# Kernel optimization log

Hardware: AMD Instinct MI355X
Metric: run time of the kernel (lower is better)

The kernel has to match this reference:

```python
import jax, jax.numpy as jnp
import numpy as np

T, N, E = 8, 20000, 320000
D_IN, H, OUT = 64, 128, 2
EPS = 1e-5  # BatchNorm eps


def setup_inputs() -> dict:
    key = jax.random.key(0)
    ks = jax.random.split(key, 24)
    rn = lambda k, shape: jax.random.normal(k, shape, jnp.float32) * 0.05
    inp = {
        "x_seq": jax.random.normal(ks[0], (T, N, D_IN), jnp.float32),
        "edge_index_seq": jax.random.randint(ks[1], (T, 2, E), 0, N),
        # GCN layer 1 (D_IN -> H) + BatchNorm (eval mode: running stats)
        "W1": rn(ks[2], (D_IN, H)), "b1": jnp.zeros((H,), jnp.float32),
        "g1": jnp.ones((H,), jnp.float32), "be1": jnp.zeros((H,), jnp.float32),
        "m1": rn(ks[3], (H,)), "v1": jax.random.uniform(ks[4], (H,), jnp.float32, 0.5, 1.5),
        # GCN layer 2 (H -> H) + BatchNorm
        "W2": rn(ks[5], (H, H)), "b2": jnp.zeros((H,), jnp.float32),
        "g2": jnp.ones((H,), jnp.float32), "be2": jnp.zeros((H,), jnp.float32),
        "m2": rn(ks[6], (H,)), "v2": jax.random.uniform(ks[7], (H,), jnp.float32, 0.5, 1.5),
        # LSTM layer 0 (PyTorch layout: W_ih [4H, in], W_hh [4H, H], gate order i,f,g,o)
        "Wih0": rn(ks[8], (4 * H, H)), "Whh0": rn(ks[9], (4 * H, H)),
        "bih0": jnp.zeros((4 * H,), jnp.float32), "bhh0": jnp.zeros((4 * H,), jnp.float32),
        # LSTM layer 1
        "Wih1": rn(ks[10], (4 * H, H)), "Whh1": rn(ks[11], (4 * H, H)),
        "bih1": jnp.zeros((4 * H,), jnp.float32), "bhh1": jnp.zeros((4 * H,), jnp.float32),
        # final classifier
        "Wc": rn(ks[12], (OUT, H)), "bc": jnp.zeros((OUT,), jnp.float32),
    }
    return inp


def gcn_conv(x, src, dst, W, b):
    # GCNConv: D^{-1/2}(A+I)D^{-1/2} X W + b, self-loops added
    n = x.shape[0]
    h = x @ W                                   # [N, F_out]
    loop = jnp.arange(n)
    s = jnp.concatenate([src, loop])
    d = jnp.concatenate([dst, loop])
    deg = jax.ops.segment_sum(jnp.ones(d.shape, x.dtype), d, num_segments=n)
    dinv = jax.lax.rsqrt(deg)                   # deg >= 1 (self-loops)
    coef = dinv[s] * dinv[d]                    # [E+N]
    agg = jax.ops.segment_sum(h[s] * coef[:, None], d, num_segments=n)
    return agg + b


def batchnorm_eval(x, g, b, m, v):
    return (x - m) * jax.lax.rsqrt(v + EPS) * g + b


def lstm_layer(xs, Wih, Whh, b):
    # xs: [T, in]; returns (ys [T,H], h_T [H])
    h0 = jnp.zeros((Whh.shape[1],), xs.dtype)

    def step(carry, xt):
        h, c = carry
        gates = xt @ Wih.T + h @ Whh.T + b
        i, f, g, o = jnp.split(gates, 4, axis=-1)
        c = jax.nn.sigmoid(f) * c + jax.nn.sigmoid(i) * jnp.tanh(g)
        h = jax.nn.sigmoid(o) * jnp.tanh(c)
        return (h, c), h

    (hT, _), ys = jax.lax.scan(step, (h0, h0), xs)
    return ys, hT


def reference(x_seq, edge_index_seq, W1, b1, g1, be1, m1, v1,
              W2, b2, g2, be2, m2, v2,
              Wih0, Whh0, bih0, bhh0, Wih1, Whh1, bih1, bhh1, Wc, bc):
    def per_t(x, e):
        src, dst = e[0], e[1]
        h = gcn_conv(x, src, dst, W1, b1)
        h = jax.nn.relu(batchnorm_eval(h, g1, be1, m1, v1))
        h = gcn_conv(h, src, dst, W2, b2)
        h = batchnorm_eval(h, g2, be2, m2, v2)
        return h.mean(axis=0)                   # global mean pool (batch=None)

    emb = jax.vmap(per_t)(x_seq, edge_index_seq)  # [T, H]
    ys, _ = lstm_layer(emb, Wih0, Whh0, bih0 + bhh0)
    _, hT = lstm_layer(ys, Wih1, Whh1, bih1 + bhh1)
    out = hT @ Wc.T + bc                          # [OUT]
    return (out[None, :], hT[None, :])
```

## Files before the change

kernel.cpp:

```cpp
#include <hip/hip_runtime.h>
#include <hip/hip_fp16.h>
#include <math.h>

#define T 8
#define N 20000
#define E 320000
#define EPS 1e-5f
#define NBA 32
#define CHUNKA 10000
#define NPACK 10000
#define NPACK4 5000
#define TILES_PT 1250
#define BW 625
#define NBUK 32
#define SPAN_MAX 13824
#define CSGRID 157
#define CVTBLK 2500

typedef _Float16 f16x8 __attribute__((ext_vector_type(8)));
typedef float f32x4 __attribute__((ext_vector_type(4)));
struct h2x2 { __half2 lo, hi; };

__device__ __forceinline__ float sigm(float x) { return 1.0f / (1.0f + expf(-x)); }

__global__ __launch_bounds__(1024) void k_partA(const int* __restrict__ edges,
                                                unsigned int* __restrict__ hist_g,
                                                unsigned int* __restrict__ bpart,
                                                int* __restrict__ bcnt) {
    __shared__ unsigned int arr[CHUNKA];
    __shared__ int cnt[NBUK], cur[NBUK];
    const int t = blockIdx.x & 7, b = blockIdx.x >> 3;
    const int tid = threadIdx.x;
    const int* keys = edges + (size_t)t * 2 * E + E + b * CHUNKA;
    const int* pays = edges + (size_t)t * 2 * E + b * CHUNKA;
    for (int i = tid; i < NPACK4; i += 1024) arr[i] = 0;
    if (tid < NBUK) cnt[tid] = 0;
    __syncthreads();
    for (int i = tid; i < CHUNKA; i += 1024) {
        int k = keys[i];
        atomicAdd(&arr[k >> 2], 1u << ((k & 3) * 8));
        atomicAdd(&cnt[k / BW], 1);
    }
    __syncthreads();
    unsigned int* hout = hist_g + (size_t)(t * NBA + b) * NPACK4;
    for (int i = tid; i < NPACK4; i += 1024) hout[i] = arr[i];
    if (tid == 0) {
        int run = 0;
        for (int u = 0; u < NBUK; u++) { cur[u] = run; run += cnt[u]; }
    }
    if (tid < NBUK) bcnt[(t * NBUK + tid) * NBUK + b] = cnt[tid];
    __syncthreads();
    for (int i = tid; i < CHUNKA; i += 1024) {
        int k = keys[i];
        int p = pays[i];
        int slot = atomicAdd(&cur[k / BW], 1);
        arr[slot] = ((unsigned int)k << 15) | (unsigned int)p;
    }
    __syncthreads();
    unsigned int* outp = bpart + (size_t)(t * NBUK + b) * CHUNKA;
    for (int i = tid; i < CHUNKA; i += 1024) outp[i] = arr[i];
}

__global__ __launch_bounds__(256) void k_colsum(
    const unsigned int* __restrict__ hist_g,
    int* __restrict__ dega, float* __restrict__ dinv,
    const float* __restrict__ W1, __half* __restrict__ W1t,
    float* __restrict__ pooled) {
    const int bid = blockIdx.x, tid = threadIdx.x;
    if (bid >= CSGRID) {
        int i = (bid - CSGRID) * 256 + tid;
        int j = i & 127, k = i >> 7;
        W1t[j * 64 + k] = __float2half(W1[i]);
        if (bid == CSGRID) {
            f32x4 z = {0.f, 0.f, 0.f, 0.f};
            ((f32x4*)pooled)[tid] = z;
        }
        return;
    }
    int idx = bid * 256 + tid;
    if (idx >= T * NPACK4) return;
    int t = idx / NPACK4, i = idx - t * NPACK4;
    const unsigned int* hp = hist_g + (size_t)t * NBA * NPACK4 + i;
    unsigned int a0 = 0, a1 = 0, a2 = 0, a3 = 0;
#pragma unroll
    for (int b = 0; b < NBA; b++) {
        unsigned int h = hp[(size_t)b * NPACK4];
        a0 += h & 0xffu; a1 += (h >> 8) & 0xffu;
        a2 += (h >> 16) & 0xffu; a3 += h >> 24;
    }
    int4 dd; dd.x = (int)a0; dd.y = (int)a1; dd.z = (int)a2; dd.w = (int)a3;
    ((int4*)dega)[idx] = dd;
    float4 df;
    df.x = rsqrtf((float)a0 + 1.0f); df.y = rsqrtf((float)a1 + 1.0f);
    df.z = rsqrtf((float)a2 + 1.0f); df.w = rsqrtf((float)a3 + 1.0f);
    ((float4*)dinv)[idx] = df;
}

__global__ __launch_bounds__(1024) void k_scanN(const int* __restrict__ dega,
                                                int* __restrict__ offs) {
    const int t = blockIdx.x, tid = threadIdx.x;
    __shared__ int sh[1024];
    int local[20];
    int sum = 0;
    if (tid < 1000) {
        const int* tp = dega + t * N + tid * 20;
#pragma unroll
        for (int i = 0; i < 20; i++) { local[i] = tp[i]; sum += local[i]; }
    }
    sh[tid] = sum;
    __syncthreads();
    for (int off = 1; off < 1024; off <<= 1) {
        int v = (tid >= off) ? sh[tid - off] : 0;
        __syncthreads();
        sh[tid] += v;
        __syncthreads();
    }
    if (tid < 1000) {
        int run = t * E + sh[tid] - sum;
        int* op = offs + t * N + tid * 20;
#pragma unroll
        for (int i = 0; i < 20; i++) { op[i] = run; run += local[i]; }
    }
    if (t == T - 1 && tid == 0) offs[T * N] = T * E;
}

__global__ __launch_bounds__(1024) void k_pw(const unsigned int* __restrict__ bpart,
                                             const int* __restrict__ bcnt,
                                             const int* __restrict__ offs,
                                             const float* __restrict__ dinv,
                                             int* __restrict__ eidx,
                                             float* __restrict__ wpart,
                                             const float* __restrict__ x,
                                             __half* __restrict__ xh) {
    __shared__ int sbuf[SPAN_MAX];
    __shared__ int cursor[BW];
    __shared__ int offb[NBUK], lenb[NBUK];
    const int bid = blockIdx.x;
    const int tid = threadIdx.x;
    if (bid >= 2 * T * NBUK) {
        int idx = (bid - 2 * T * NBUK) * 1024 + tid;
        if (idx >= T * N * 16) return;
        if (idx < 16) {
            ushort4 z; z.x = 0; z.y = 0; z.z = 0; z.w = 0;
            ((ushort4*)(xh + (size_t)T * N * 64))[idx] = z;
        }
        float d = dinv[idx >> 4];
        f32x4 vv = __builtin_nontemporal_load((const f32x4*)x + idx);
        __half h0 = __float2half(vv.x * d);
        __half h1 = __float2half(vv.y * d);
        __half h2 = __float2half(vv.z * d);
        __half h3 = __float2half(vv.w * d);
        ushort4 pack;
        pack.x = *(unsigned short*)&h0;
        pack.y = *(unsigned short*)&h1;
        pack.z = *(unsigned short*)&h2;
        pack.w = *(unsigned short*)&h3;
        ((ushort4*)xh)[idx] = pack;
        return;
    }
    if (bid >= T * NBUK) {
        float* wf = (float*)sbuf;
        const int bb = bid - T * NBUK;
        const int t = bb & 7, b = bb >> 3;
        const unsigned int* run = bpart + (size_t)(t * NBUK + b) * CHUNKA;
        const float* dv = dinv + t * N;
        for (int half = 0; half < 2; half++) {
            for (int i = tid; i < NPACK; i += 1024) wf[i] = 0.f;
            __syncthreads();
            int lo = half * NPACK;
            for (int i = tid; i < CHUNKA; i += 1024) {
                unsigned int it = run[i];
                int q = (int)(it & 0x7fffu) - lo;
                if (q >= 0 && q < NPACK) atomicAdd(&wf[q], dv[it >> 15]);
            }
            __syncthreads();
            float* out = wpart + (size_t)(t * NBUK + b) * N + lo;
            for (int i = tid; i < NPACK; i += 1024) out[i] = wf[i];
            __syncthreads();
        }
        return;
    }
    const int t = bid & 7, u = bid >> 3;
    const int nodeBase = t * N + u * BW;
    const int dstBase = u * BW;
    const int segStart = offs[nodeBase];
    const int segEnd = offs[nodeBase + BW];
    const int span = segEnd - segStart;
    if (tid < NBUK) {
        int s = 0;
        for (int uu = 0; uu < u; uu++) s += bcnt[(t * NBUK + uu) * NBUK + tid];
        offb[tid] = s;
        lenb[tid] = bcnt[(t * NBUK + u) * NBUK + tid];
    }
    for (int j = tid; j < BW; j += 1024) cursor[j] = offs[nodeBase + j] - segStart;
    __syncthreads();
    if (span <= SPAN_MAX) {
        for (int b = 0; b < NBUK; b++) {
            const unsigned int* src = bpart + (size_t)(t * NBUK + b) * CHUNKA + offb[b];
            int len = lenb[b];
            for (int i = tid; i < len; i += 1024) {
                unsigned int it = src[i];
                int pos = atomicAdd(&cursor[(int)(it >> 15) - dstBase], 1);
                sbuf[pos] = (int)(it & 0x7fffu) << 4;
            }
            __syncthreads();
        }
        int* out = eidx + segStart;
        for (int i = tid; i < span; i += 1024) out[i] = sbuf[i];
    } else {
        for (int b = 0; b < NBUK; b++) {
            const unsigned int* src = bpart + (size_t)(t * NBUK + b) * CHUNKA + offb[b];
            int len = lenb[b];
            for (int i = tid; i < len; i += 1024) {
                unsigned int it = src[i];
                int pos = atomicAdd(&cursor[(int)(it >> 15) - dstBase], 1);
                eidx[segStart + pos] = (int)(it & 0x7fffu) << 4;
            }
            __syncthreads();
        }
    }
}

__global__ __launch_bounds__(256) void k_gather(
    const int* __restrict__ eidx, const int* __restrict__ offs,
    const float* __restrict__ dinv, const __half* __restrict__ xh,
    __half* __restrict__ vh) {
    const int t = blockIdx.x & 7;
    const int n = ((blockIdx.x >> 3) << 2) + (threadIdx.x >> 6);
    const int lane = threadIdx.x & 63;
    const int q = lane & 15, s = lane >> 4;
    if (n >= N) return;
    const int node = t * N + n;
    const int start = offs[node];
    const int end = offs[node + 1];
    const h2x2* xt4 = (const h2x2*)(xh + (size_t)t * N * 64);
    const int zrow = (T - t) * (N * 16);
    float a0 = 0.f, a1 = 0.f, a2 = 0.f, a3 = 0.f;
    for (int bs = start; bs < end; bs += 64) {
        int cnt = end - bs; if (cnt > 64) cnt = 64;
        int idx = zrow;
        if (lane < cnt) idx = __builtin_nontemporal_load(&eidx[bs + lane]);
        __half2 hlo = __float2half2_rn(0.f);
        __half2 hhi = __float2half2_rn(0.f);
        for (int e = 0; e < cnt; e += 16) {
            int o0 = __shfl(idx, e + s),      o1 = __shfl(idx, e + 4 + s);
            int o2 = __shfl(idx, e + 8 + s),  o3 = __shfl(idx, e + 12 + s);
            h2x2 v0 = xt4[o0 + q], v1 = xt4[o1 + q];
            h2x2 v2 = xt4[o2 + q], v3 = xt4[o3 + q];
            __half2 p01l = __hadd2(v0.lo, v1.lo), p23l = __hadd2(v2.lo, v3.lo);
            __half2 p01h = __hadd2(v0.hi, v1.hi), p23h = __hadd2(v2.hi, v3.hi);
            hlo = __hadd2(hlo, __hadd2(p01l, p23l));
            hhi = __hadd2(hhi, __hadd2(p01h, p23h));
        }
        float2 flo = __half22float2(hlo), fhi = __half22float2(hhi);
        a0 += flo.x; a1 += flo.y; a2 += fhi.x; a3 += fhi.y;
    }
    a0 += __shfl_xor(a0, 16); a1 += __shfl_xor(a1, 16);
    a2 += __shfl_xor(a2, 16); a3 += __shfl_xor(a3, 16);
    a0 += __shfl_xor(a0, 32); a1 += __shfl_xor(a1, 32);
    a2 += __shfl_xor(a2, 32); a3 += __shfl_xor(a3, 32);
    if (s == 0) {
        float di = dinv[node];
        h2x2 self = xt4[(n << 4) + q];
        float2 sl = __half22float2(self.lo), sh = __half22float2(self.hi);
        float r0 = di * (a0 + sl.x), r1 = di * (a1 + sl.y);
        float r2 = di * (a2 + sh.x), r3 = di * (a3 + sh.y);
        h2x2 outp;
        outp.lo = __floats2half2_rn(r0, r1);
        outp.hi = __floats2half2_rn(r2, r3);
        ((h2x2*)vh)[(size_t)node * 16 + q] = outp;
    }
}

__global__ __launch_bounds__(256) void k_mfma_pool(
    const __half* __restrict__ vh, const float* __restrict__ wpart,
    const float* __restrict__ dinv, const __half* __restrict__ W1t,
    const float* __restrict__ b1, const float* __restrict__ g1,
    const float* __restrict__ be1, const float* __restrict__ m1,
    const float* __restrict__ v1, float* __restrict__ pooled) {
    const int t = blockIdx.x & 7;
    const int bt = blockIdx.x >> 3;
    const int w = threadIdx.x >> 6, lane = threadIdx.x & 63;
    const int q = lane >> 4, col = lane & 15;
    const size_t tb = (size_t)t * N;

    f16x8 bfr[8][2];
    float sbv[8], stv[8];
#pragma unroll
    for (int jt = 0; jt < 8; jt++) {
        int j = jt * 16 + col;
        float s = g1[j] * rsqrtf(v1[j] + EPS);
        sbv[jt] = s;
        stv[jt] = s * b1[j] + be1[j] - m1[j] * s;
#pragma unroll
        for (int kk = 0; kk < 2; kk++)
            bfr[jt][kk] = *(const f16x8*)(W1t + (size_t)j * 64 + kk * 32 + q * 8);
    }
    float pool8[8];
#pragma unroll
    for (int jt = 0; jt < 8; jt++) pool8[jt] = 0.f;

    for (int i = 0; i < 8; i++) {
        int tau = bt * 32 + w * 8 + i;
        if (tau >= TILES_PT) break;
        int nb = tau * 16;
        const __half* vrow = vh + (tb + nb + col) * 64;
        f16x8 a0 = *(const f16x8*)(vrow + q * 8);
        f16x8 a1 = *(const f16x8*)(vrow + 32 + q * 8);
        float4 dv = ((const float4*)(dinv + tb + nb))[q];
        float4 sv = {0.f, 0.f, 0.f, 0.f};
#pragma unroll 8
        for (int b = 0; b < NBUK; b++) {
            float4 wv = ((const float4*)(wpart + (size_t)(t * NBUK + b) * N + nb))[q];
            sv.x += wv.x; sv.y += wv.y; sv.z += wv.z; sv.w += wv.w;
        }
        float4 af;
        af.x = dv.x * (sv.x + dv.x);
        af.y = dv.y * (sv.y + dv.y);
        af.z = dv.z * (sv.z + dv.z);
        af.w = dv.w * (sv.w + dv.w);
#pragma unroll
        for (int jt = 0; jt < 8; jt++) {
            f32x4 acc = {0.f, 0.f, 0.f, 0.f};
            acc = __builtin_amdgcn_mfma_f32_16x16x32_f16(a0, bfr[jt][0], acc, 0, 0, 0);
            acc = __builtin_amdgcn_mfma_f32_16x16x32_f16(a1, bfr[jt][1], acc, 0, 0, 0);
            float s = sbv[jt], sh = stv[jt];
            pool8[jt] += fmaxf(s * acc[0] + sh, 0.f) * af.x
                       + fmaxf(s * acc[1] + sh, 0.f) * af.y
                       + fmaxf(s * acc[2] + sh, 0.f) * af.z
                       + fmaxf(s * acc[3] + sh, 0.f) * af.w;
        }
    }
#pragma unroll
    for (int jt = 0; jt < 8; jt++) {
        pool8[jt] += __shfl_xor(pool8[jt], 16);
        pool8[jt] += __shfl_xor(pool8[jt], 32);
    }
    if (lane < 16) {
#pragma unroll
        for (int jt = 0; jt < 8; jt++)
            atomicAdd(&pooled[t * 128 + jt * 16 + lane], pool8[jt]);
    }
}

__global__ __launch_bounds__(512) void k_emb(
    const float* __restrict__ pooled,
    const float* __restrict__ W2, const float* __restrict__ b2,
    const float* __restrict__ g2, const float* __restrict__ be2,
    const float* __restrict__ m2, const float* __restrict__ v2,
    const float* __restrict__ Wih0, const float* __restrict__ bih0,
    const float* __restrict__ bhh0, float* __restrict__ gx0_g,
    const float* __restrict__ Whh0, const float* __restrict__ Whh1,
    const float* __restrict__ Wih1,
    __half* __restrict__ Whh0h, __half* __restrict__ Whh1h,
    __half* __restrict__ Wih1h) {
    const int tid = threadIdx.x;
    if (blockIdx.x >= T) {
        int wb = blockIdx.x - T;
        const float* src; __half* dst;
        if (wb < 16)      { src = Whh0; dst = Whh0h; }
        else if (wb < 32) { src = Whh1; dst = Whh1h; wb -= 16; }
        else              { src = Wih1; dst = Wih1h; wb -= 32; }
        int off = wb * 4096;
        for (int i = off + tid; i < off + 4096; i += 512)
            dst[i] = __float2half(src[i]);
        return;
    }
    const int t = blockIdx.x;
    __shared__ float pm[128];
    __shared__ float es[128];
    if (tid < 128) pm[tid] = pooled[t * 128 + tid] * (1.0f / N);
    __syncthreads();
    if (tid < 128) {
        float s = g2[tid] * rsqrtf(v2[tid] + EPS);
        float sh = be2[tid] - m2[tid] * s;
        float dot = 0.f;
#pragma unroll 8
        for (int k = 0; k < 128; k++) dot += pm[k] * W2[k * 128 + tid];
        es[tid] = s * (dot + b2[tid]) + sh;
    }
    __syncthreads();
    float dot = bih0[tid] + bhh0[tid];
    const float4* w = (const float4*)(Wih0 + tid * 128);
    const float4* e4 = (const float4*)es;
#pragma unroll
    for (int k4 = 0; k4 < 32; k4++) {
        float4 a = w[k4], bb = e4[k4];
        dot += a.x * bb.x + a.y * bb.y + a.z * bb.z + a.w * bb.w;
    }
    gx0_g[t * 512 + tid] = dot;
}

__global__ __launch_bounds__(1024) void k_head2(
    const float* __restrict__ gx0_g,
    const __half* __restrict__ Whh0h, const __half* __restrict__ Wih1h,
    const __half* __restrict__ Whh1h,
    const float* __restrict__ bih1, const float* __restrict__ bhh1,
    const float* __restrict__ Wc, const float* __restrict__ bc,
    float* __restrict__ out) {
    __shared__ float gx[T][512];
    __shared__ float ys[T][128];
    __shared__ float h[128];
    __shared__ float part[1024];
    const int tid = threadIdx.x;
    const int r = tid & 511, hf = tid >> 9;
    float c = 0.f;
    for (int i = tid; i < T * 512; i += 1024) gx[i >> 9][i & 511] = gx0_g[i];
    if (tid < 128) h[tid] = 0.f;
    __syncthreads();
    {
        const h2x2* wrow = (const h2x2*)(Whh0h + r * 128 + hf * 64);
        for (int t = 0; t < T; t++) {
            const float4* h4 = ((const float4*)h) + hf * 16;
            float dot = 0.f;
#pragma unroll
            for (int k = 0; k < 16; k++) {
                h2x2 wv = wrow[k];
                float4 hv = h4[k];
                float2 wl = __half22float2(wv.lo), wh = __half22float2(wv.hi);
                dot += wl.x * hv.x + wl.y * hv.y + wh.x * hv.z + wh.y * hv.w;
            }
            part[tid] = dot;
            __syncthreads();
            if (tid < 128) {
                float i_ = gx[t][tid]       + part[tid]       + part[512 + tid];
                float f_ = gx[t][128 + tid] + part[128 + tid] + part[640 + tid];
                float g_ = gx[t][256 + tid] + part[256 + tid] + part[768 + tid];
                float o_ = gx[t][384 + tid] + part[384 + tid] + part[896 + tid];
                c = sigm(f_) * c + sigm(i_) * tanhf(g_);
                float hv = sigm(o_) * tanhf(c);
                h[tid] = hv;
                ys[t][tid] = hv;
            }
            __syncthreads();
        }
    }
    {
        const h2x2* wrow = (const h2x2*)(Wih1h + r * 128 + hf * 64);
        float bias = (hf == 0) ? (bih1[r] + bhh1[r]) : 0.f;
        for (int t = 0; t < T; t++) {
            const float4* y4 = ((const float4*)ys[t]) + hf * 16;
            float dot = bias;
#pragma unroll
            for (int k = 0; k < 16; k++) {
                h2x2 wv = wrow[k];
                float4 yv = y4[k];
                float2 wl = __half22float2(wv.lo), wh = __half22float2(wv.hi);
                dot += wl.x * yv.x + wl.y * yv.y + wh.x * yv.z + wh.y * yv.w;
            }
            part[tid] = dot;
            __syncthreads();
            if (tid < 512) gx[t][tid] = part[tid] + part[512 + tid];
            __syncthreads();
        }
    }
    if (tid < 128) h[tid] = 0.f;
    c = 0.f;
    __syncthreads();
    {
        const h2x2* wrow = (const h2x2*)(Whh1h + r * 128 + hf * 64);
        for (int t = 0; t < T; t++) {
            const float4* h4 = ((const float4*)h) + hf * 16;
            float dot = 0.f;
#pragma unroll
            for (int k = 0; k < 16; k++) {
                h2x2 wv = wrow[k];
                float4 hv = h4[k];
                float2 wl = __half22float2(wv.lo), wh = __half22float2(wv.hi);
                dot += wl.x * hv.x + wl.y * hv.y + wh.x * hv.z + wh.y * hv.w;
            }
            part[tid] = dot;
            __syncthreads();
            if (tid < 128) {
                float i_ = gx[t][tid]       + part[tid]       + part[512 + tid];
                float f_ = gx[t][128 + tid] + part[128 + tid] + part[640 + tid];
                float g_ = gx[t][256 + tid] + part[256 + tid] + part[768 + tid];
                float o_ = gx[t][384 + tid] + part[384 + tid] + part[896 + tid];
                c = sigm(f_) * c + sigm(i_) * tanhf(g_);
                h[tid] = sigm(o_) * tanhf(c);
            }
            __syncthreads();
        }
    }
    if (tid < 2) {
        float dot = bc[tid];
#pragma unroll 8
        for (int k = 0; k < 128; k++) dot += h[k] * Wc[tid * 128 + k];
        out[tid] = dot;
    }
    if (tid < 128) out[2 + tid] = h[tid];
}

extern "C" void kernel_launch(void* const* d_in, const int* in_sizes, int n_in,
                              void* d_out, int out_size, void* d_ws, size_t ws_size,
                              hipStream_t stream) {
    const float* x    = (const float*)d_in[0];
    const int*   edges= (const int*)d_in[1];
    const float* W1   = (const float*)d_in[2];
    const float* b1   = (const float*)d_in[3];
    const float* g1   = (const float*)d_in[4];
    const float* be1  = (const float*)d_in[5];
    const float* m1   = (const float*)d_in[6];
    const float* v1   = (const float*)d_in[7];
    const float* W2   = (const float*)d_in[8];
    const float* b2   = (const float*)d_in[9];
    const float* g2   = (const float*)d_in[10];
    const float* be2  = (const float*)d_in[11];
    const float* m2   = (const float*)d_in[12];
    const float* v2   = (const float*)d_in[13];
    const float* Wih0 = (const float*)d_in[14];
    const float* Whh0 = (const float*)d_in[15];
    const float* bih0 = (const float*)d_in[16];
    const float* bhh0 = (const float*)d_in[17];
    const float* Wih1 = (const float*)d_in[18];
    const float* Whh1 = (const float*)d_in[19];
    const float* bih1 = (const float*)d_in[20];
    const float* bhh1 = (const float*)d_in[21];
    const float* Wc   = (const float*)d_in[22];
    const float* bc   = (const float*)d_in[23];

    char* base = (char*)d_ws;
    unsigned int* hist_g = (unsigned int*)base;
    unsigned int* bpart  = (unsigned int*)(base + (size_t)T * NBA * NPACK * 4);
    __half*       vh     = (__half*)base;
    char* p = base + (size_t)T * NBA * NPACK * 4 + (size_t)T * NBUK * CHUNKA * 4;
    __half* xh    = (__half*)p;             p += (size_t)T * N * 64 * 2 + 128;
    int*   offs   = (int*)p;                p += (size_t)(T * N + 1) * 4 + 12;
    int*   dega   = (int*)p;                p += (size_t)T * N * 4;
    float* dinv   = (float*)p;              p += (size_t)T * N * 4;
    __half* Whh0h = (__half*)p;             p += (size_t)65536 * 2;
    __half* Whh1h = (__half*)p;             p += (size_t)65536 * 2;
    __half* Wih1h = (__half*)p;             p += (size_t)65536 * 2;
    float* gx0_g  = (float*)p;              p += (size_t)T * 512 * 4;
    int*   eidx   = (int*)p;                p += (size_t)T * E * 4;
    float* wpart  = (float*)p;              p += (size_t)T * NBUK * N * 4;
    int*   bcnt   = (int*)p;                p += (size_t)T * NBUK * NBUK * 4;
    float* pooled = (float*)p;              p += (size_t)T * 128 * 4;
    __half* W1t   = (__half*)p;

    k_partA<<<T * NBUK, 1024, 0, stream>>>(edges, hist_g, bpart, bcnt);
    k_colsum<<<CSGRID + 32, 256, 0, stream>>>(hist_g, dega, dinv, W1, W1t, pooled);
    k_scanN<<<T, 1024, 0, stream>>>(dega, offs);
    k_pw<<<2 * T * NBUK + CVTBLK, 1024, 0, stream>>>(bpart, bcnt, offs, dinv,
                                                     eidx, wpart, x, xh);
    k_gather<<<(T * N) / 4, 256, 0, stream>>>(eidx, offs, dinv, xh, vh);
    k_mfma_pool<<<8 * 40, 256, 0, stream>>>(vh, wpart, dinv, W1t, b1, g1, be1, m1, v1, pooled);
    k_emb<<<T + 48, 512, 0, stream>>>(pooled, W2, b2, g2, be2, m2, v2,
                                      Wih0, bih0, bhh0, gx0_g,
                                      Whh0, Whh1, Wih1, Whh0h, Whh1h, Wih1h);
    k_head2<<<1, 1024, 0, stream>>>(gx0_g, Whh0h, Wih1h, Whh1h,
                                    bih1, bhh1, Wc, bc, (float*)d_out);
}
```

Measured before the change: 344.5 us.

## Fuse all pipeline stages into one cooperative persistent kernel with grid syncs

Eight separate kernel launches are merged into one cooperative kernel of 256 blocks of 1024 threads. The stages are separated by grid.sync() calls and share memory through a union. The aim is to remove launch overheads and the gaps between kernels. In exchange, later stages such as gather and MFMA pooling that used many small blocks are now restricted to 256 large blocks. That could reduce occupancy and parallelism, and the grid barriers have their own cost.

```diff
diff --git a/kernel.cpp b/kernel.cpp
--- a/kernel.cpp
+++ b/kernel.cpp
@@ -1,6 +1,9 @@
 #include <hip/hip_runtime.h>
 #include <hip/hip_fp16.h>
+#include <hip/hip_cooperative_groups.h>
 #include <math.h>
+
+namespace cg = cooperative_groups;
 
 #define T 8
 #define N 20000
@@ -14,8 +17,6 @@
 #define BW 625
 #define NBUK 32
 #define SPAN_MAX 13824
-#define CSGRID 157
-#define CVTBLK 2500
 
 typedef _Float16 f16x8 __attribute__((ext_vector_type(8)));
 typedef float f32x4 __attribute__((ext_vector_type(4)));
@@ -23,147 +24,181 @@
 
 __device__ __forceinline__ float sigm(float x) { return 1.0f / (1.0f + expf(-x)); }
 
-__global__ __launch_bounds__(1024) void k_partA(const int* __restrict__ edges,
-                                                unsigned int* __restrict__ hist_g,
-                                                unsigned int* __restrict__ bpart,
-                                                int* __restrict__ bcnt) {
-    __shared__ unsigned int arr[CHUNKA];
-    __shared__ int cnt[NBUK], cur[NBUK];
-    const int t = blockIdx.x & 7, b = blockIdx.x >> 3;
-    const int tid = threadIdx.x;
-    const int* keys = edges + (size_t)t * 2 * E + E + b * CHUNKA;
-    const int* pays = edges + (size_t)t * 2 * E + b * CHUNKA;
-    for (int i = tid; i < NPACK4; i += 1024) arr[i] = 0;
-    if (tid < NBUK) cnt[tid] = 0;
-    __syncthreads();
-    for (int i = tid; i < CHUNKA; i += 1024) {
-        int k = keys[i];
-        atomicAdd(&arr[k >> 2], 1u << ((k & 3) * 8));
-        atomicAdd(&cnt[k / BW], 1);
-    }
-    __syncthreads();
-    unsigned int* hout = hist_g + (size_t)(t * NBA + b) * NPACK4;
-    for (int i = tid; i < NPACK4; i += 1024) hout[i] = arr[i];
-    if (tid == 0) {
-        int run = 0;
-        for (int u = 0; u < NBUK; u++) { cur[u] = run; run += cnt[u]; }
-    }
-    if (tid < NBUK) bcnt[(t * NBUK + tid) * NBUK + b] = cnt[tid];
-    __syncthreads();
-    for (int i = tid; i < CHUNKA; i += 1024) {
-        int k = keys[i];
-        int p = pays[i];
-        int slot = atomicAdd(&cur[k / BW], 1);
-        arr[slot] = ((unsigned int)k << 15) | (unsigned int)p;
-    }
-    __syncthreads();
-    unsigned int* outp = bpart + (size_t)(t * NBUK + b) * CHUNKA;
-    for (int i = tid; i < CHUNKA; i += 1024) outp[i] = arr[i];
-}
-
-__global__ __launch_bounds__(256) void k_colsum(
-    const unsigned int* __restrict__ hist_g,
-    int* __restrict__ dega, float* __restrict__ dinv,
-    const float* __restrict__ W1, __half* __restrict__ W1t,
-    float* __restrict__ pooled) {
-    const int bid = blockIdx.x, tid = threadIdx.x;
-    if (bid >= CSGRID) {
-        int i = (bid - CSGRID) * 256 + tid;
-        int j = i & 127, k = i >> 7;
-        W1t[j * 64 + k] = __float2half(W1[i]);
-        if (bid == CSGRID) {
-            f32x4 z = {0.f, 0.f, 0.f, 0.f};
-            ((f32x4*)pooled)[tid] = z;
-        }
-        return;
-    }
-    int idx = bid * 256 + tid;
-    if (idx >= T * NPACK4) return;
-    int t = idx / NPACK4, i = idx - t * NPACK4;
-    const unsigned int* hp = hist_g + (size_t)t * NBA * NPACK4 + i;
-    unsigned int a0 = 0, a1 = 0, a2 = 0, a3 = 0;
-#pragma unroll
-    for (int b = 0; b < NBA; b++) {
-        unsigned int h = hp[(size_t)b * NPACK4];
-        a0 += h & 0xffu; a1 += (h >> 8) & 0xffu;
-        a2 += (h >> 16) & 0xffu; a3 += h >> 24;
-    }
-    int4 dd; dd.x = (int)a0; dd.y = (int)a1; dd.z = (int)a2; dd.w = (int)a3;
-    ((int4*)dega)[idx] = dd;
-    float4 df;
-    df.x = rsqrtf((float)a0 + 1.0f); df.y = rsqrtf((float)a1 + 1.0f);
-    df.z = rsqrtf((float)a2 + 1.0f); df.w = rsqrtf((float)a3 + 1.0f);
-    ((float4*)dinv)[idx] = df;
-}
-
-__global__ __launch_bounds__(1024) void k_scanN(const int* __restrict__ dega,
-                                                int* __restrict__ offs) {
-    const int t = blockIdx.x, tid = threadIdx.x;
-    __shared__ int sh[1024];
-    int local[20];
-    int sum = 0;
-    if (tid < 1000) {
-        const int* tp = dega + t * N + tid * 20;
-#pragma unroll
-        for (int i = 0; i < 20; i++) { local[i] = tp[i]; sum += local[i]; }
-    }
-    sh[tid] = sum;
-    __syncthreads();
-    for (int off = 1; off < 1024; off <<= 1) {
-        int v = (tid >= off) ? sh[tid - off] : 0;
-        __syncthreads();
-        sh[tid] += v;
-        __syncthreads();
-    }
-    if (tid < 1000) {
-        int run = t * E + sh[tid] - sum;
-        int* op = offs + t * N + tid * 20;
-#pragma unroll
-        for (int i = 0; i < 20; i++) { op[i] = run; run += local[i]; }
-    }
-    if (t == T - 1 && tid == 0) offs[T * N] = T * E;
-}
-
-__global__ __launch_bounds__(1024) void k_pw(const unsigned int* __restrict__ bpart,
-                                             const int* __restrict__ bcnt,
-                                             const int* __restrict__ offs,
-                                             const float* __restrict__ dinv,
-                                             int* __restrict__ eidx,
-                                             float* __restrict__ wpart,
-                                             const float* __restrict__ x,
-                                             __half* __restrict__ xh) {
-    __shared__ int sbuf[SPAN_MAX];
-    __shared__ int cursor[BW];
-    __shared__ int offb[NBUK], lenb[NBUK];
+struct P {
+    const float *x; const int *edges;
+    const float *W1,*b1,*g1,*be1,*m1,*v1,*W2,*b2,*g2,*be2,*m2,*v2;
+    const float *Wih0,*Whh0,*bih0,*bhh0,*Wih1,*Whh1,*bih1,*bhh1,*Wc,*bc;
+    unsigned int *hist_g,*bpart; int *bcnt,*dega; float *dinv;
+    int *offs,*eidx; float *wpart,*alpha; __half *xh,*vh,*W1t;
+    float *pooled,*gx0_g; __half *Whh0h,*Whh1h,*Wih1h; float *out;
+};
+
+union SmemU {
+    struct { unsigned int arr[CHUNKA]; int cnt[NBUK]; int cur[NBUK]; } a;
+    struct { int sbuf[SPAN_MAX]; int cursor[BW]; int offb[NBUK]; int lenb[NBUK]; } d;
+    struct { int sh[1024]; } c;
+    struct { float pm[128]; float es[128]; } g8;
+    struct { float gx[T][512]; float ys[T][128]; float h[128]; float part[1024]; } h8;
+};
+
+__global__ __launch_bounds__(1024, 4) void k_all(P p) {
+    cg::grid_group grid = cg::this_grid();
+    __shared__ SmemU sm;
     const int bid = blockIdx.x;
     const int tid = threadIdx.x;
-    if (bid >= 2 * T * NBUK) {
-        int idx = (bid - 2 * T * NBUK) * 1024 + tid;
-        if (idx >= T * N * 16) return;
-        if (idx < 16) {
-            ushort4 z; z.x = 0; z.y = 0; z.z = 0; z.w = 0;
-            ((ushort4*)(xh + (size_t)T * N * 64))[idx] = z;
-        }
-        float d = dinv[idx >> 4];
-        f32x4 vv = __builtin_nontemporal_load((const f32x4*)x + idx);
-        __half h0 = __float2half(vv.x * d);
-        __half h1 = __float2half(vv.y * d);
-        __half h2 = __float2half(vv.z * d);
-        __half h3 = __float2half(vv.w * d);
-        ushort4 pack;
-        pack.x = *(unsigned short*)&h0;
-        pack.y = *(unsigned short*)&h1;
-        pack.z = *(unsigned short*)&h2;
-        pack.w = *(unsigned short*)&h3;
-        ((ushort4*)xh)[idx] = pack;
-        return;
-    }
-    if (bid >= T * NBUK) {
-        float* wf = (float*)sbuf;
-        const int bb = bid - T * NBUK;
-        const int t = bb & 7, b = bb >> 3;
-        const unsigned int* run = bpart + (size_t)(t * NBUK + b) * CHUNKA;
-        const float* dv = dinv + t * N;
+
+    {
+        const int t = bid & 7, b = bid >> 3;
+        const int* keys = p.edges + (size_t)t * 2 * E + E + b * CHUNKA;
+        const int* pays = p.edges + (size_t)t * 2 * E + b * CHUNKA;
+        for (int i = tid; i < NPACK4; i += 1024) sm.a.arr[i] = 0;
+        if (tid < NBUK) sm.a.cnt[tid] = 0;
+        __syncthreads();
+        for (int i = tid; i < CHUNKA; i += 1024) {
+            int k = keys[i];
+            atomicAdd(&sm.a.arr[k >> 2], 1u << ((k & 3) * 8));
+            atomicAdd(&sm.a.cnt[k / BW], 1);
+        }
+        __syncthreads();
+        unsigned int* hout = p.hist_g + (size_t)(t * NBA + b) * NPACK4;
+        for (int i = tid; i < NPACK4; i += 1024) hout[i] = sm.a.arr[i];
+        if (tid == 0) {
+            int run = 0;
+            for (int u = 0; u < NBUK; u++) { sm.a.cur[u] = run; run += sm.a.cnt[u]; }
+        }
+        if (tid < NBUK) p.bcnt[(t * NBUK + tid) * NBUK + b] = sm.a.cnt[tid];
+        __syncthreads();
+        for (int i = tid; i < CHUNKA; i += 1024) {
+            int k = keys[i];
+            int pp = pays[i];
+            int slot = atomicAdd(&sm.a.cur[k / BW], 1);
+            sm.a.arr[slot] = ((unsigned int)k << 15) | (unsigned int)pp;
+        }
+        __syncthreads();
+        unsigned int* outp = p.bpart + (size_t)(t * NBUK + b) * CHUNKA;
+        for (int i = tid; i < CHUNKA; i += 1024) outp[i] = sm.a.arr[i];
+    }
+    grid.sync();
+
+    {
+        int g = bid * 1024 + tid;
+        if (g < T * NPACK4) {
+            int t = g / NPACK4, i = g - t * NPACK4;
+            const unsigned int* hp = p.hist_g + (size_t)t * NBA * NPACK4 + i;
+            unsigned int a0 = 0, a1 = 0, a2 = 0, a3 = 0;
+#pragma unroll
+            for (int b = 0; b < NBA; b++) {
+                unsigned int h = hp[(size_t)b * NPACK4];
+                a0 += h & 0xffu; a1 += (h >> 8) & 0xffu;
+                a2 += (h >> 16) & 0xffu; a3 += h >> 24;
+            }
+            int4 dd; dd.x = (int)a0; dd.y = (int)a1; dd.z = (int)a2; dd.w = (int)a3;
+            ((int4*)p.dega)[g] = dd;
+            float4 df;
+            df.x = rsqrtf((float)a0 + 1.0f); df.y = rsqrtf((float)a1 + 1.0f);
+            df.z = rsqrtf((float)a2 + 1.0f); df.w = rsqrtf((float)a3 + 1.0f);
+            ((float4*)p.dinv)[g] = df;
+        } else if (g < T * NPACK4 + 8192) {
+            int i = g - T * NPACK4;
+            int j = i & 127, k = i >> 7;
+            p.W1t[j * 64 + k] = __float2half(p.W1[i]);
+        } else if (g < T * NPACK4 + 8192 + 256) {
+            f32x4 z = {0.f, 0.f, 0.f, 0.f};
+            ((f32x4*)p.pooled)[g - T * NPACK4 - 8192] = z;
+        }
+    }
+    grid.sync();
+
+    if (bid < T) {
+        const int t = bid;
+        int local[20];
+        int sum = 0;
+        if (tid < 1000) {
+            const int* tp = p.dega + t * N + tid * 20;
+#pragma unroll
+            for (int i = 0; i < 20; i++) { local[i] = tp[i]; sum += local[i]; }
+        }
+        sm.c.sh[tid] = sum;
+        __syncthreads();
+        for (int off = 1; off < 1024; off <<= 1) {
+            int v = (tid >= off) ? sm.c.sh[tid - off] : 0;
+            __syncthreads();
+            sm.c.sh[tid] += v;
+            __syncthreads();
+        }
+        if (tid < 1000) {
+            int run = t * E + sm.c.sh[tid] - sum;
+            int* op = p.offs + t * N + tid * 20;
+#pragma unroll
+            for (int i = 0; i < 20; i++) { op[i] = run; run += local[i]; }
+        }
+        if (t == T - 1 && tid == 0) p.offs[T * N] = T * E;
+    } else {
+        for (int idx = (bid - T) * 1024 + tid; idx < T * N * 16; idx += (256 - T) * 1024) {
+            if (idx < 16) {
+                ushort4 z; z.x = 0; z.y = 0; z.z = 0; z.w = 0;
+                ((ushort4*)(p.xh + (size_t)T * N * 64))[idx] = z;
+            }
+            float d = p.dinv[idx >> 4];
+            f32x4 vv = __builtin_nontemporal_load((const f32x4*)p.x + idx);
+            __half h0 = __float2half(vv.x * d);
+            __half h1 = __float2half(vv.y * d);
+            __half h2 = __float2half(vv.z * d);
+            __half h3 = __float2half(vv.w * d);
+            ushort4 pack;
+            pack.x = *(unsigned short*)&h0;
+            pack.y = *(unsigned short*)&h1;
+            pack.z = *(unsigned short*)&h2;
+            pack.w = *(unsigned short*)&h3;
+            ((ushort4*)p.xh)[idx] = pack;
+        }
+    }
+    grid.sync();
+
+    {
+        const int t = bid & 7, u = bid >> 3;
+        const int nodeBase = t * N + u * BW;
+        const int dstBase = u * BW;
+        const int segStart = p.offs[nodeBase];
+        const int segEnd = p.offs[nodeBase + BW];
+        const int span = segEnd - segStart;
+        if (tid < NBUK) {
+            int s = 0;
+            for (int uu = 0; uu < u; uu++) s += p.bcnt[(t * NBUK + uu) * NBUK + tid];
+            sm.d.offb[tid] = s;
+            sm.d.lenb[tid] = p.bcnt[(t * NBUK + u) * NBUK + tid];
+        }
+        for (int j = tid; j < BW; j += 1024) sm.d.cursor[j] = p.offs[nodeBase + j] - segStart;
+        __syncthreads();
+        if (span <= SPAN_MAX) {
+            for (int b = 0; b < NBUK; b++) {
+                const unsigned int* src = p.bpart + (size_t)(t * NBUK + b) * CHUNKA + sm.d.offb[b];
+                int len = sm.d.lenb[b];
+                for (int i = tid; i < len; i += 1024) {
+                    unsigned int it = src[i];
+                    int pos = atomicAdd(&sm.d.cursor[(int)(it >> 15) - dstBase], 1);
+                    sm.d.sbuf[pos] = (int)(it & 0x7fffu) << 4;
+                }
+                __syncthreads();
+            }
+            int* out = p.eidx + segStart;
+            for (int i = tid; i < span; i += 1024) out[i] = sm.d.sbuf[i];
+        } else {
+            for (int b = 0; b < NBUK; b++) {
+                const unsigned int* src = p.bpart + (size_t)(t * NBUK + b) * CHUNKA + sm.d.offb[b];
+                int len = sm.d.lenb[b];
+                for (int i = tid; i < len; i += 1024) {
+                    unsigned int it = src[i];
+                    int pos = atomicAdd(&sm.d.cursor[(int)(it >> 15) - dstBase], 1);
+                    p.eidx[segStart + pos] = (int)(it & 0x7fffu) << 4;
+                }
+                __syncthreads();
+            }
+        }
+        __syncthreads();
+        float* wf = (float*)sm.d.sbuf;
+        const unsigned int* run = p.bpart + (size_t)(t * NBUK + u) * CHUNKA;
+        const float* dv = p.dinv + t * N;
         for (int half = 0; half < 2; half++) {
             for (int i = tid; i < NPACK; i += 1024) wf[i] = 0.f;
             __syncthreads();
@@ -174,380 +209,303 @@
                 if (q >= 0 && q < NPACK) atomicAdd(&wf[q], dv[it >> 15]);
             }
             __syncthreads();
-            float* out = wpart + (size_t)(t * NBUK + b) * N + lo;
+            float* out = p.wpart + (size_t)(t * NBUK + u) * N + lo;
             for (int i = tid; i < NPACK; i += 1024) out[i] = wf[i];
             __syncthreads();
         }
-        return;
-    }
-    const int t = bid & 7, u = bid >> 3;
-    const int nodeBase = t * N + u * BW;
-    const int dstBase = u * BW;
-    const int segStart = offs[nodeBase];
-    const int segEnd = offs[nodeBase + BW];
-    const int span = segEnd - segStart;
-    if (tid < NBUK) {
-        int s = 0;
-        for (int uu = 0; uu < u; uu++) s += bcnt[(t * NBUK + uu) * NBUK + tid];
-        offb[tid] = s;
-        lenb[tid] = bcnt[(t * NBUK + u) * NBUK + tid];
-    }
-    for (int j = tid; j < BW; j += 1024) cursor[j] = offs[nodeBase + j] - segStart;
-    __syncthreads();
-    if (span <= SPAN_MAX) {
-        for (int b = 0; b < NBUK; b++) {
-            const unsigned int* src = bpart + (size_t)(t * NBUK + b) * CHUNKA + offb[b];
-            int len = lenb[b];
-            for (int i = tid; i < len; i += 1024) {
-                unsigned int it = src[i];
-                int pos = atomicAdd(&cursor[(int)(it >> 15) - dstBase], 1);
-                sbuf[pos] = (int)(it & 0x7fffu) << 4;
-            }
-            __syncthreads();
-        }
-        int* out = eidx + segStart;
-        for (int i = tid; i < span; i += 1024) out[i] = sbuf[i];
-    } else {
-        for (int b = 0; b < NBUK; b++) {
-            const unsigned int* src = bpart + (size_t)(t * NBUK + b) * CHUNKA + offb[b];
-            int len = lenb[b];
-            for (int i = tid; i < len; i += 1024) {
-                unsigned int it = src[i];
-                int pos = atomicAdd(&cursor[(int)(it >> 15) - dstBase], 1);
-                eidx[segStart + pos] = (int)(it & 0x7fffu) << 4;
-            }
-            __syncthreads();
-        }
-    }
-}
-
-__global__ __launch_bounds__(256) void k_gather(
-    const int* __restrict__ eidx, const int* __restrict__ offs,
-    const float* __restrict__ dinv, const __half* __restrict__ xh,
-    __half* __restrict__ vh) {
-    const int t = blockIdx.x & 7;
-    const int n = ((blockIdx.x >> 3) << 2) + (threadIdx.x >> 6);
-    const int lane = threadIdx.x & 63;
-    const int q = lane & 15, s = lane >> 4;
-    if (n >= N) return;
-    const int node = t * N + n;
-    const int start = offs[node];
-    const int end = offs[node + 1];
-    const h2x2* xt4 = (const h2x2*)(xh + (size_t)t * N * 64);
-    const int zrow = (T - t) * (N * 16);
-    float a0 = 0.f, a1 = 0.f, a2 = 0.f, a3 = 0.f;
-    for (int bs = start; bs < end; bs += 64) {
-        int cnt = end - bs; if (cnt > 64) cnt = 64;
-        int idx = zrow;
-        if (lane < cnt) idx = __builtin_nontemporal_load(&eidx[bs + lane]);
-        __half2 hlo = __float2half2_rn(0.f);
-        __half2 hhi = __float2half2_rn(0.f);
-        for (int e = 0; e < cnt; e += 16) {
-            int o0 = __shfl(idx, e + s),      o1 = __shfl(idx, e + 4 + s);
-            int o2 = __shfl(idx, e + 8 + s),  o3 = __shfl(idx, e + 12 + s);
-            h2x2 v0 = xt4[o0 + q], v1 = xt4[o1 + q];
-            h2x2 v2 = xt4[o2 + q], v3 = xt4[o3 + q];
-            __half2 p01l = __hadd2(v0.lo, v1.lo), p23l = __hadd2(v2.lo, v3.lo);
-            __half2 p01h = __hadd2(v0.hi, v1.hi), p23h = __hadd2(v2.hi, v3.hi);
-            hlo = __hadd2(hlo, __hadd2(p01l, p23l));
-            hhi = __hadd2(hhi, __hadd2(p01h, p23h));
-        }
-        float2 flo = __half22float2(hlo), fhi = __half22float2(hhi);
-        a0 += flo.x; a1 += flo.y; a2 += fhi.x; a3 += fhi.y;
-    }
-    a0 += __shfl_xor(a0, 16); a1 += __shfl_xor(a1, 16);
-    a2 += __shfl_xor(a2, 16); a3 += __shfl_xor(a3, 16);
-    a0 += __shfl_xor(a0, 32); a1 += __shfl_xor(a1, 32);
-    a2 += __shfl_xor(a2, 32); a3 += __shfl_xor(a3, 32);
-    if (s == 0) {
-        float di = dinv[node];
-        h2x2 self = xt4[(n << 4) + q];
-        float2 sl = __half22float2(self.lo), sh = __half22float2(self.hi);
-        float r0 = di * (a0 + sl.x), r1 = di * (a1 + sl.y);
-        float r2 = di * (a2 + sh.x), r3 = di * (a3 + sh.y);
-        h2x2 outp;
-        outp.lo = __floats2half2_rn(r0, r1);
-        outp.hi = __floats2half2_rn(r2, r3);
-        ((h2x2*)vh)[(size_t)node * 16 + q] = outp;
-    }
-}
-
-__global__ __launch_bounds__(256) void k_mfma_pool(
-    const __half* __restrict__ vh, const float* __restrict__ wpart,
-    const float* __restrict__ dinv, const __half* __restrict__ W1t,
-    const float* __restrict__ b1, const float* __restrict__ g1,
-    const float* __restrict__ be1, const float* __restrict__ m1,
-    const float* __restrict__ v1, float* __restrict__ pooled) {
-    const int t = blockIdx.x & 7;
-    const int bt = blockIdx.x >> 3;
-    const int w = threadIdx.x >> 6, lane = threadIdx.x & 63;
-    const int q = lane >> 4, col = lane & 15;
-    const size_t tb = (size_t)t * N;
-
-    f16x8 bfr[8][2];
-    float sbv[8], stv[8];
-#pragma unroll
-    for (int jt = 0; jt < 8; jt++) {
-        int j = jt * 16 + col;
-        float s = g1[j] * rsqrtf(v1[j] + EPS);
-        sbv[jt] = s;
-        stv[jt] = s * b1[j] + be1[j] - m1[j] * s;
-#pragma unroll
-        for (int kk = 0; kk < 2; kk++)
-            bfr[jt][kk] = *(const f16x8*)(W1t + (size_t)j * 64 + kk * 32 + q * 8);
-    }
-    float pool8[8];
-#pragma unroll
-    for (int jt = 0; jt < 8; jt++) pool8[jt] = 0.f;
-
-    for (int i = 0; i < 8; i++) {
-        int tau = bt * 32 + w * 8 + i;
-        if (tau >= TILES_PT) break;
-        int nb = tau * 16;
-        const __half* vrow = vh + (tb + nb + col) * 64;
-        f16x8 a0 = *(const f16x8*)(vrow + q * 8);
-        f16x8 a1 = *(const f16x8*)(vrow + 32 + q * 8);
-        float4 dv = ((const float4*)(dinv + tb + nb))[q];
-        float4 sv = {0.f, 0.f, 0.f, 0.f};
+    }
+    grid.sync();
+
+    {
+        int g = bid * 1024 + tid;
+        if (g < T * N) {
+            int t = g / N, n = g - t * N;
+            float s = 0.f;
+#pragma unroll
+            for (int b = 0; b < NBUK; b++) s += p.wpart[(size_t)(t * NBUK + b) * N + n];
+            float di = p.dinv[g];
+            p.alpha[g] = di * (s + di);
+        }
+    }
+    {
+        const int t = bid & 7;
+        const int wv = tid >> 6, lane = tid & 63;
+        const int wtid = (bid >> 3) * 16 + wv;
+        const int q = lane & 15, s = lane >> 4;
+        const h2x2* xt4 = (const h2x2*)(p.xh + (size_t)t * N * 64);
+        const int zrow = (T - t) * (N * 16);
+        for (int n = wtid; n < N; n += 512) {
+            const int node = t * N + n;
+            const int st = p.offs[node];
+            const int en = p.offs[node + 1];
+            float a0 = 0.f, a1 = 0.f, a2 = 0.f, a3 = 0.f;
+            for (int bs = st; bs < en; bs += 64) {
+                int cnt = en - bs; if (cnt > 64) cnt = 64;
+                int idx = zrow;
+                if (lane < cnt) idx = __builtin_nontemporal_load(&p.eidx[bs + lane]);
+                __half2 hlo = __float2half2_rn(0.f);
+                __half2 hhi = __float2half2_rn(0.f);
+                for (int e = 0; e < cnt; e += 16) {
+                    int o0 = __shfl(idx, e + s),      o1 = __shfl(idx, e + 4 + s);
+                    int o2 = __shfl(idx, e + 8 + s),  o3 = __shfl(idx, e + 12 + s);
+                    h2x2 v0 = xt4[o0 + q], v1 = xt4[o1 + q];
+                    h2x2 v2 = xt4[o2 + q], v3 = xt4[o3 + q];
+                    __half2 p01l = __hadd2(v0.lo, v1.lo), p23l = __hadd2(v2.lo, v3.lo);
+                    __half2 p01h = __hadd2(v0.hi, v1.hi), p23h = __hadd2(v2.hi, v3.hi);
+                    hlo = __hadd2(hlo, __hadd2(p01l, p23l));
+                    hhi = __hadd2(hhi, __hadd2(p01h, p23h));
+                }
+                float2 flo = __half22float2(hlo), fhi = __half22float2(hhi);
+                a0 += flo.x; a1 += flo.y; a2 += fhi.x; a3 += fhi.y;
+            }
+            a0 += __shfl_xor(a0, 16); a1 += __shfl_xor(a1, 16);
+            a2 += __shfl_xor(a2, 16); a3 += __shfl_xor(a3, 16);
+            a0 += __shfl_xor(a0, 32); a1 += __shfl_xor(a1, 32);
+            a2 += __shfl_xor(a2, 32); a3 += __shfl_xor(a3, 32);
+            if (s == 0) {
+                float di = p.dinv[node];
+                h2x2 self = xt4[(n << 4) + q];
+                float2 sl = __half22float2(self.lo), sh = __half22float2(self.hi);
+                float r0 = di * (a0 + sl.x), r1 = di * (a1 + sl.y);
+                float r2 = di * (a2 + sh.x), r3 = di * (a3 + sh.y);
+                h2x2 outp;
+                outp.lo = __floats2half2_rn(r0, r1);
+                outp.hi = __floats2half2_rn(r2, r3);
+                ((h2x2*)p.vh)[(size_t)node * 16 + q] = outp;
+            }
+        }
+    }
+    grid.sync();
+
+    {
+        const int t = bid & 7;
+        const int wv = tid >> 6, lane = tid & 63;
+        const int wtid = (bid >> 3) * 16 + wv;
+        const int q4 = lane >> 4, col = lane & 15;
+        const size_t tb = (size_t)t * N;
+        f16x8 bfr[8][2];
+        float sbv[8], stv[8];
+#pragma unroll
+        for (int jt = 0; jt < 8; jt++) {
+            int j = jt * 16 + col;
+            float sc = p.g1[j] * rsqrtf(p.v1[j] + EPS);
+            sbv[jt] = sc;
+            stv[jt] = sc * p.b1[j] + p.be1[j] - p.m1[j] * sc;
+#pragma unroll
+            for (int kk = 0; kk < 2; kk++)
+                bfr[jt][kk] = *(const f16x8*)(p.W1t + (size_t)j * 64 + kk * 32 + q4 * 8);
+        }
+        float pool8[8];
+#pragma unroll
+        for (int jt = 0; jt < 8; jt++) pool8[jt] = 0.f;
+        for (int tau = wtid; tau < TILES_PT; tau += 512) {
+            int nb = tau * 16;
+            const __half* vrow = p.vh + (tb + nb + col) * 64;
+            f16x8 a0 = *(const f16x8*)(vrow + q4 * 8);
+            f16x8 a1 = *(const f16x8*)(vrow + 32 + q4 * 8);
+            float4 af = ((const float4*)(p.alpha + tb + nb))[q4];
+#pragma unroll
+            for (int jt = 0; jt < 8; jt++) {
+                f32x4 acc = {0.f, 0.f, 0.f, 0.f};
+                acc = __builtin_amdgcn_mfma_f32_16x16x32_f16(a0, bfr[jt][0], acc, 0, 0, 0);
+                acc = __builtin_amdgcn_mfma_f32_16x16x32_f16(a1, bfr[jt][1], acc, 0, 0, 0);
+                float sc = sbv[jt], sh = stv[jt];
+                pool8[jt] += fmaxf(sc * acc[0] + sh, 0.f) * af.x
+                           + fmaxf(sc * acc[1] + sh, 0.f) * af.y
+                           + fmaxf(sc * acc[2] + sh, 0.f) * af.z
+                           + fmaxf(sc * acc[3] + sh, 0.f) * af.w;
+            }
+        }
+#pragma unroll
+        for (int jt = 0; jt < 8; jt++) {
+            pool8[jt] += __shfl_xor(pool8[jt], 16);
+            pool8[jt] += __shfl_xor(pool8[jt], 32);
+        }
+        if (lane < 16) {
+#pragma unroll
+            for (int jt = 0; jt < 8; jt++)
+                atomicAdd(&p.pooled[t * 128 + jt * 16 + lane], pool8[jt]);
+        }
+    }
+    grid.sync();
+
+    if (bid < T) {
+        const int t = bid;
+        if (tid < 128) sm.g8.pm[tid] = p.pooled[t * 128 + tid] * (1.0f / N);
+        __syncthreads();
+        if (tid < 128) {
+            float sc = p.g2[tid] * rsqrtf(p.v2[tid] + EPS);
+            float sh = p.be2[tid] - p.m2[tid] * sc;
+            float dot = 0.f;
 #pragma unroll 8
-        for (int b = 0; b < NBUK; b++) {
-            float4 wv = ((const float4*)(wpart + (size_t)(t * NBUK + b) * N + nb))[q];
-            sv.x += wv.x; sv.y += wv.y; sv.z += wv.z; sv.w += wv.w;
-        }
-        float4 af;
-        af.x = dv.x * (sv.x + dv.x);
-        af.y = dv.y * (sv.y + dv.y);
-        af.z = dv.z * (sv.z + dv.z);
-        af.w = dv.w * (sv.w + dv.w);
-#pragma unroll
-        for (int jt = 0; jt < 8; jt++) {
-            f32x4 acc = {0.f, 0.f, 0.f, 0.f};
-            acc = __builtin_amdgcn_mfma_f32_16x16x32_f16(a0, bfr[jt][0], acc, 0, 0, 0);
-            acc = __builtin_amdgcn_mfma_f32_16x16x32_f16(a1, bfr[jt][1], acc, 0, 0, 0);
-            float s = sbv[jt], sh = stv[jt];
-            pool8[jt] += fmaxf(s * acc[0] + sh, 0.f) * af.x
-                       + fmaxf(s * acc[1] + sh, 0.f) * af.y
-                       + fmaxf(s * acc[2] + sh, 0.f) * af.z
-                       + fmaxf(s * acc[3] + sh, 0.f) * af.w;
-        }
-    }
-#pragma unroll
-    for (int jt = 0; jt < 8; jt++) {
-        pool8[jt] += __shfl_xor(pool8[jt], 16);
-        pool8[jt] += __shfl_xor(pool8[jt], 32);
-    }
-    if (lane < 16) {
-#pragma unroll
-        for (int jt = 0; jt < 8; jt++)
-            atomicAdd(&pooled[t * 128 + jt * 16 + lane], pool8[jt]);
-    }
-}
-
-__global__ __launch_bounds__(512) void k_emb(
-    const float* __restrict__ pooled,
-    const float* __restrict__ W2, const float* __restrict__ b2,
-    const float* __restrict__ g2, const float* __restrict__ be2,
-    const float* __restrict__ m2, const float* __restrict__ v2,
-    const float* __restrict__ Wih0, const float* __restrict__ bih0,
-    const float* __restrict__ bhh0, float* __restrict__ gx0_g,
-    const float* __restrict__ Whh0, const float* __restrict__ Whh1,
-    const float* __restrict__ Wih1,
-    __half* __restrict__ Whh0h, __half* __restrict__ Whh1h,
-    __half* __restrict__ Wih1h) {
-    const int tid = threadIdx.x;
-    if (blockIdx.x >= T) {
-        int wb = blockIdx.x - T;
+            for (int k = 0; k < 128; k++) dot += sm.g8.pm[k] * p.W2[k * 128 + tid];
+            sm.g8.es[tid] = sc * (dot + p.b2[tid]) + sh;
+        }
+        __syncthreads();
+        if (tid < 512) {
+            float dot = p.bih0[tid] + p.bhh0[tid];
+            const float4* w = (const float4*)(p.Wih0 + tid * 128);
+            const float4* e4 = (const float4*)sm.g8.es;
+#pragma unroll
+            for (int k4 = 0; k4 < 32; k4++) {
+                float4 a = w[k4], bb = e4[k4];
+                dot += a.x * bb.x + a.y * bb.y + a.z * bb.z + a.w * bb.w;
+            }
+            p.gx0_g[t * 512 + tid] = dot;
+        }
+    } else if (bid < T + 48) {
+        int wb = bid - T;
         const float* src; __half* dst;
-        if (wb < 16)      { src = Whh0; dst = Whh0h; }
-        else if (wb < 32) { src = Whh1; dst = Whh1h; wb -= 16; }
-        else              { src = Wih1; dst = Wih1h; wb -= 32; }
+        if (wb < 16)      { src = p.Whh0; dst = p.Whh0h; }
+        else if (wb < 32) { src = p.Whh1; dst = p.Whh1h; wb -= 16; }
+        else              { src = p.Wih1; dst = p.Wih1h; wb -= 32; }
         int off = wb * 4096;
-        for (int i = off + tid; i < off + 4096; i += 512)
+        for (int i = off + tid; i < off + 4096; i += 1024)
             dst[i] = __float2half(src[i]);
-        return;
-    }
-    const int t = blockIdx.x;
-    __shared__ float pm[128];
-    __shared__ float es[128];
-    if (tid < 128) pm[tid] = pooled[t * 128 + tid] * (1.0f / N);
-    __syncthreads();
-    if (tid < 128) {
-        float s = g2[tid] * rsqrtf(v2[tid] + EPS);
-        float sh = be2[tid] - m2[tid] * s;
-        float dot = 0.f;
+    }
+    grid.sync();
+
+    if (bid == 0) {
+        const int r = tid & 511, hf = tid >> 9;
+        float c = 0.f;
+        for (int i = tid; i < T * 512; i += 1024) sm.h8.gx[i >> 9][i & 511] = p.gx0_g[i];
+        if (tid < 128) sm.h8.h[tid] = 0.f;
+        __syncthreads();
+        {
+            const h2x2* wrow = (const h2x2*)(p.Whh0h + r * 128 + hf * 64);
+            for (int t = 0; t < T; t++) {
+                const float4* h4 = ((const float4*)sm.h8.h) + hf * 16;
+                float dot = 0.f;
+#pragma unroll
+                for (int k = 0; k < 16; k++) {
+                    h2x2 wv = wrow[k];
+                    float4 hv = h4[k];
+                    float2 wl = __half22float2(wv.lo), wh = __half22float2(wv.hi);
+                    dot += wl.x * hv.x + wl.y * hv.y + wh.x * hv.z + wh.y * hv.w;
+                }
+                sm.h8.part[tid] = dot;
+                __syncthreads();
+                if (tid < 128) {
+                    float i_ = sm.h8.gx[t][tid]       + sm.h8.part[tid]       + sm.h8.part[512 + tid];
+                    float f_ = sm.h8.gx[t][128 + tid] + sm.h8.part[128 + tid] + sm.h8.part[640 + tid];
+                    float g_ = sm.h8.gx[t][256 + tid] + sm.h8.part[256 + tid] + sm.h8.part[768 + tid];
+                    float o_ = sm.h8.gx[t][384 + tid] + sm.h8.part[384 + tid] + sm.h8.part[896 + tid];
+                    c = sigm(f_) * c + sigm(i_) * tanhf(g_);
+                    float hv = sigm(o_) * tanhf(c);
+                    sm.h8.h[tid] = hv;
+                    sm.h8.ys[t][tid] = hv;
+                }
+                __syncthreads();
+            }
+        }
+        {
+            const h2x2* wrow = (const h2x2*)(p.Wih1h + r * 128 + hf * 64);
+            float bias = (hf == 0) ? (p.bih1[r] + p.bhh1[r]) : 0.f;
+            for (int t = 0; t < T; t++) {
+                const float4* y4 = ((const float4*)sm.h8.ys[t]) + hf * 16;
+                float dot = bias;
+#pragma unroll
+                for (int k = 0; k < 16; k++) {
+                    h2x2 wv = wrow[k];
+                    float4 yv = y4[k];
+                    float2 wl = __half22float2(wv.lo), wh = __half22float2(wv.hi);
+                    dot += wl.x * yv.x + wl.y * yv.y + wh.x * yv.z + wh.y * yv.w;
+                }
+                sm.h8.part[tid] = dot;
+                __syncthreads();
+                if (tid < 512) sm.h8.gx[t][tid] = sm.h8.part[tid] + sm.h8.part[512 + tid];
+                __syncthreads();
+            }
+        }
+        if (tid < 128) sm.h8.h[tid] = 0.f;
+        c = 0.f;
+        __syncthreads();
+        {
+            const h2x2* wrow = (const h2x2*)(p.Whh1h + r * 128 + hf * 64);
+            for (int t = 0; t < T; t++) {
+                const float4* h4 = ((const float4*)sm.h8.h) + hf * 16;
+                float dot = 0.f;
+#pragma unroll
+                for (int k = 0; k < 16; k++) {
+                    h2x2 wv = wrow[k];
+                    float4 hv = h4[k];
+                    float2 wl = __half22float2(wv.lo), wh = __half22float2(wv.hi);
+                    dot += wl.x * hv.x + wl.y * hv.y + wh.x * hv.z + wh.y * hv.w;
+                }
+                sm.h8.part[tid] = dot;
+                __syncthreads();
+                if (tid < 128) {
+                    float i_ = sm.h8.gx[t][tid]       + sm.h8.part[tid]       + sm.h8.part[512 + tid];
+                    float f_ = sm.h8.gx[t][128 + tid] + sm.h8.part[128 + tid] + sm.h8.part[640 + tid];
+                    float g_ = sm.h8.gx[t][256 + tid] + sm.h8.part[256 + tid] + sm.h8.part[768 + tid];
+                    float o_ = sm.h8.gx[t][384 + tid] + sm.h8.part[384 + tid] + sm.h8.part[896 + tid];
+                    c = sigm(f_) * c + sigm(i_) * tanhf(g_);
+                    sm.h8.h[tid] = sigm(o_) * tanhf(c);
+                }
+                __syncthreads();
+            }
+        }
+        if (tid < 2) {
+            float dot = p.bc[tid];
 #pragma unroll 8
-        for (int k = 0; k < 128; k++) dot += pm[k] * W2[k * 128 + tid];
-        es[tid] = s * (dot + b2[tid]) + sh;
-    }
-    __syncthreads();
-    float dot = bih0[tid] + bhh0[tid];
-    const float4* w = (const float4*)(Wih0 + tid * 128);
-    const float4* e4 = (const float4*)es;
-#pragma unroll
-    for (int k4 = 0; k4 < 32; k4++) {
-        float4 a = w[k4], bb = e4[k4];
-        dot += a.x * bb.x + a.y * bb.y + a.z * bb.z + a.w * bb.w;
-    }
-    gx0_g[t * 512 + tid] = dot;
-}
-
-__global__ __launch_bounds__(1024) void k_head2(
-    const float* __restrict__ gx0_g,
-    const __half* __restrict__ Whh0h, const __half* __restrict__ Wih1h,
-    const __half* __restrict__ Whh1h,
-    const float* __restrict__ bih1, const float* __restrict__ bhh1,
-    const float* __restrict__ Wc, const float* __restrict__ bc,
-    float* __restrict__ out) {
-    __shared__ float gx[T][512];
-    __shared__ float ys[T][128];
-    __shared__ float h[128];
-    __shared__ float part[1024];
-    const int tid = threadIdx.x;
-    const int r = tid & 511, hf = tid >> 9;
-    float c = 0.f;
-    for (int i = tid; i < T * 512; i += 1024) gx[i >> 9][i & 511] = gx0_g[i];
-    if (tid < 128) h[tid] = 0.f;
-    __syncthreads();
-    {
-        const h2x2* wrow = (const h2x2*)(Whh0h + r * 128 + hf * 64);
-        for (int t = 0; t < T; t++) {
-            const float4* h4 = ((const float4*)h) + hf * 16;
-            float dot = 0.f;
-#pragma unroll
-            for (int k = 0; k < 16; k++) {
-                h2x2 wv = wrow[k];
-                float4 hv = h4[k];
-                float2 wl = __half22float2(wv.lo), wh = __half22float2(wv.hi);
-                dot += wl.x * hv.x + wl.y * hv.y + wh.x * hv.z + wh.y * hv.w;
-            }
-            part[tid] = dot;
-            __syncthreads();
-            if (tid < 128) {
-                float i_ = gx[t][tid]       + part[tid]       + part[512 + tid];
-                float f_ = gx[t][128 + tid] + part[128 + tid] + part[640 + tid];
-                float g_ = gx[t][256 + tid] + part[256 + tid] + part[768 + tid];
-                float o_ = gx[t][384 + tid] + part[384 + tid] + part[896 + tid];
-                c = sigm(f_) * c + sigm(i_) * tanhf(g_);
-                float hv = sigm(o_) * tanhf(c);
-                h[tid] = hv;
-                ys[t][tid] = hv;
-            }
-            __syncthreads();
-        }
-    }
-    {
-        const h2x2* wrow = (const h2x2*)(Wih1h + r * 128 + hf * 64);
-        float bias = (hf == 0) ? (bih1[r] + bhh1[r]) : 0.f;
-        for (int t = 0; t < T; t++) {
-            const float4* y4 = ((const float4*)ys[t]) + hf * 16;
-            float dot = bias;
-#pragma unroll
-            for (int k = 0; k < 16; k++) {
-                h2x2 wv = wrow[k];
-                float4 yv = y4[k];
-                float2 wl = __half22float2(wv.lo), wh = __half22float2(wv.hi);
-                dot += wl.x * yv.x + wl.y * yv.y + wh.x * yv.z + wh.y * yv.w;
-            }
-            part[tid] = dot;
-            __syncthreads();
-            if (tid < 512) gx[t][tid] = part[tid] + part[512 + tid];
-            __syncthreads();
-        }
-    }
-    if (tid < 128) h[tid] = 0.f;
-    c = 0.f;
-    __syncthreads();
-    {
-        const h2x2* wrow = (const h2x2*)(Whh1h + r * 128 + hf * 64);
-        for (int t = 0; t < T; t++) {
-            const float4* h4 = ((const float4*)h) + hf * 16;
-            float dot = 0.f;
-#pragma unroll
-            for (int k = 0; k < 16; k++) {
-                h2x2 wv = wrow[k];
-                float4 hv = h4[k];
-                float2 wl = __half22float2(wv.lo), wh = __half22float2(wv.hi);
-                dot += wl.x * hv.x + wl.y * hv.y + wh.x * hv.z + wh.y * hv.w;
-            }
-            part[tid] = dot;
-            __syncthreads();
-            if (tid < 128) {
-                float i_ = gx[t][tid]       + part[tid]       + part[512 + tid];
-                float f_ = gx[t][128 + tid] + part[128 + tid] + part[640 + tid];
-                float g_ = gx[t][256 + tid] + part[256 + tid] + part[768 + tid];
-                float o_ = gx[t][384 + tid] + part[384 + tid] + part[896 + tid];
-                c = sigm(f_) * c + sigm(i_) * tanhf(g_);
-                h[tid] = sigm(o_) * tanhf(c);
-            }
-            __syncthreads();
-        }
-    }
-    if (tid < 2) {
-        float dot = bc[tid];
-#pragma unroll 8
-        for (int k = 0; k < 128; k++) dot += h[k] * Wc[tid * 128 + k];
-        out[tid] = dot;
-    }
-    if (tid < 128) out[2 + tid] = h[tid];
+            for (int k = 0; k < 128; k++) dot += sm.h8.h[k] * p.Wc[tid * 128 + k];
+            p.out[tid] = dot;
+        }
+        if (tid < 128) p.out[2 + tid] = sm.h8.h[tid];
+    }
 }
 
 extern "C" void kernel_launch(void* const* d_in, const int* in_sizes, int n_in,
                               void* d_out, int out_size, void* d_ws, size_t ws_size,
                               hipStream_t stream) {
-    const float* x    = (const float*)d_in[0];
-    const int*   edges= (const int*)d_in[1];
-    const float* W1   = (const float*)d_in[2];
-    const float* b1   = (const float*)d_in[3];
-    const float* g1   = (const float*)d_in[4];
-    const float* be1  = (const float*)d_in[5];
-    const float* m1   = (const float*)d_in[6];
-    const float* v1   = (const float*)d_in[7];
-    const float* W2   = (const float*)d_in[8];
-    const float* b2   = (const float*)d_in[9];
-    const float* g2   = (const float*)d_in[10];
-    const float* be2  = (const float*)d_in[11];
-    const float* m2   = (const float*)d_in[12];
-    const float* v2   = (const float*)d_in[13];
-    const float* Wih0 = (const float*)d_in[14];
-    const float* Whh0 = (const float*)d_in[15];
-    const float* bih0 = (const float*)d_in[16];
-    const float* bhh0 = (const float*)d_in[17];
-    const float* Wih1 = (const float*)d_in[18];
-    const float* Whh1 = (const float*)d_in[19];
-    const float* bih1 = (const float*)d_in[20];
-    const float* bhh1 = (const float*)d_in[21];
-    const float* Wc   = (const float*)d_in[22];
-    const float* bc   = (const float*)d_in[23];
+    P prm;
+    prm.x    = (const float*)d_in[0];
+    prm.edges= (const int*)d_in[1];
+    prm.W1   = (const float*)d_in[2];
+    prm.b1   = (const float*)d_in[3];
+    prm.g1   = (const float*)d_in[4];
+    prm.be1  = (const float*)d_in[5];
+    prm.m1   = (const float*)d_in[6];
+    prm.v1   = (const float*)d_in[7];
+    prm.W2   = (const float*)d_in[8];
+    prm.b2   = (const float*)d_in[9];
+    prm.g2   = (const float*)d_in[10];
+    prm.be2  = (const float*)d_in[11];
+    prm.m2   = (const float*)d_in[12];
+    prm.v2   = (const float*)d_in[13];
+    prm.Wih0 = (const float*)d_in[14];
+    prm.Whh0 = (const float*)d_in[15];
+    prm.bih0 = (const float*)d_in[16];
+    prm.bhh0 = (const float*)d_in[17];
+    prm.Wih1 = (const float*)d_in[18];
+    prm.Whh1 = (const float*)d_in[19];
+    prm.bih1 = (const float*)d_in[20];
+    prm.bhh1 = (const float*)d_in[21];
+    prm.Wc   = (const float*)d_in[22];
+    prm.bc   = (const float*)d_in[23];
 
     char* base = (char*)d_ws;
-    unsigned int* hist_g = (unsigned int*)base;
-    unsigned int* bpart  = (unsigned int*)(base + (size_t)T * NBA * NPACK * 4);
-    __half*       vh     = (__half*)base;
+    prm.hist_g = (unsigned int*)base;
+    prm.bpart  = (unsigned int*)(base + (size_t)T * NBA * NPACK * 4);
+    prm.vh     = (__half*)base;
     char* p = base + (size_t)T * NBA * NPACK * 4 + (size_t)T * NBUK * CHUNKA * 4;
-    __half* xh    = (__half*)p;             p += (size_t)T * N * 64 * 2 + 128;
-    int*   offs   = (int*)p;                p += (size_t)(T * N + 1) * 4 + 12;
-    int*   dega   = (int*)p;                p += (size_t)T * N * 4;
-    float* dinv   = (float*)p;              p += (size_t)T * N * 4;
-    __half* Whh0h = (__half*)p;             p += (size_t)65536 * 2;
-    __half* Whh1h = (__half*)p;             p += (size_t)65536 * 2;
-    __half* Wih1h = (__half*)p;             p += (size_t)65536 * 2;
-    float* gx0_g  = (float*)p;              p += (size_t)T * 512 * 4;
-    int*   eidx   = (int*)p;                p += (size_t)T * E * 4;
-    float* wpart  = (float*)p;              p += (size_t)T * NBUK * N * 4;
-    int*   bcnt   = (int*)p;                p += (size_t)T * NBUK * NBUK * 4;
-    float* pooled = (float*)p;              p += (size_t)T * 128 * 4;
-    __half* W1t   = (__half*)p;
-
-    k_partA<<<T * NBUK, 1024, 0, stream>>>(edges, hist_g, bpart, bcnt);
-    k_colsum<<<CSGRID + 32, 256, 0, stream>>>(hist_g, dega, dinv, W1, W1t, pooled);
-    k_scanN<<<T, 1024, 0, stream>>>(dega, offs);
-    k_pw<<<2 * T * NBUK + CVTBLK, 1024, 0, stream>>>(bpart, bcnt, offs, dinv,
-                                                     eidx, wpart, x, xh);
-    k_gather<<<(T * N) / 4, 256, 0, stream>>>(eidx, offs, dinv, xh, vh);
-    k_mfma_pool<<<8 * 40, 256, 0, stream>>>(vh, wpart, dinv, W1t, b1, g1, be1, m1, v1, pooled);
-    k_emb<<<T + 48, 512, 0, stream>>>(pooled, W2, b2, g2, be2, m2, v2,
-                                      Wih0, bih0, bhh0, gx0_g,
-                                      Whh0, Whh1, Wih1, Whh0h, Whh1h, Wih1h);
-    k_head2<<<1, 1024, 0, stream>>>(gx0_g, Whh0h, Wih1h, Whh1h,
-                                    bih1, bhh1, Wc, bc, (float*)d_out);
+    prm.xh    = (__half*)p;          p += (size_t)T * N * 64 * 2 + 128;
+    prm.offs  = (int*)p;             p += (size_t)(T * N + 1) * 4 + 12;
+    prm.dega  = (int*)p;             p += (size_t)T * N * 4;
+    prm.dinv  = (float*)p;           p += (size_t)T * N * 4;
+    prm.alpha = (float*)p;           p += (size_t)T * N * 4;
+    prm.Whh0h = (__half*)p;          p += (size_t)65536 * 2;
+    prm.Whh1h = (__half*)p;          p += (size_t)65536 * 2;
+    prm.Wih1h = (__half*)p;          p += (size_t)65536 * 2;
+    prm.gx0_g = (float*)p;           p += (size_t)T * 512 * 4;
+    prm.eidx  = (int*)p;             p += (size_t)T * E * 4;
+    prm.wpart = (float*)p;           p += (size_t)T * NBUK * N * 4;
+    prm.bcnt  = (int*)p;             p += (size_t)T * NBUK * NBUK * 4;
+    prm.pooled= (float*)p;           p += (size_t)T * 128 * 4;
+    prm.W1t   = (__half*)p;
+    prm.out   = (float*)d_out;
+
+    void* kargs[] = { (void*)&prm };
+    (void)hipLaunchCooperativeKernel((const void*)k_all, dim3(256), dim3(1024),
+                                     kargs, 0, stream);
 }
```

Result: slower. 669.6 us (+94.4%).
